# Performance work log

Hardware: AMD Instinct MI355X
Metric: run time of the kernel (lower is better)

## Reference

```python
import jax, jax.numpy as jnp
import numpy as np

B, T, D, U = 64, 128, 1024, 1024


def setup_inputs() -> dict:
    key = jax.random.key(0)
    k_x, k_r, k_s, k_wi, k_wh = jax.random.split(key, 5)
    x = jax.random.normal(k_x, (B, T, D), dtype=jnp.float32)
    reset = jax.random.randint(k_r, (B, T), 0, 2, dtype=jnp.int32)
    state = jax.random.normal(k_s, (B, T, U), dtype=jnp.float32)
    # hk.GRU params: w_i (input->3*hidden), w_h (hidden->3*hidden), bias (3*hidden)
    w_i = jax.random.normal(k_wi, (D, 3 * U), dtype=jnp.float32) * (1.0 / np.sqrt(D))
    w_h = jax.random.normal(k_wh, (U, 3 * U), dtype=jnp.float32) * (1.0 / np.sqrt(U))
    b = jnp.zeros((3 * U,), dtype=jnp.float32)
    return {"x": x, "reset": reset, "state": state, "w_i": w_i, "w_h": w_h, "b": b}


def reference(x, reset, state, w_i, w_h, b):
    # _prepare_for_rnn merges (B,T)->rows and adds a length-1 time axis, so
    # hk.dynamic_unroll(ResetCore(GRU)) == one ResetCore(GRU) step over B*T rows.
    Bd, Td, Dd = x.shape
    Ud = w_h.shape[0]
    xf = x.reshape(Bd * Td, Dd)                      # [N, D]
    h = state.reshape(Bd * Td, Ud)                   # [N, U]
    should_reset = reset.reshape(Bd * Td, 1).astype(bool)
    # hk.ResetCore: replace state with initial_state (zeros) where reset is set
    h = jnp.where(should_reset, jnp.zeros_like(h), h)
    # hk.GRU step
    gates_x = xf @ w_i                               # [N, 3U]
    zr_x, a_x = gates_x[:, : 2 * Ud], gates_x[:, 2 * Ud :]
    zr = jax.nn.sigmoid(zr_x + h @ w_h[:, : 2 * Ud] + b[: 2 * Ud])
    z, r = zr[:, :Ud], zr[:, Ud:]
    a = jnp.tanh(a_x + (r * h) @ w_h[:, 2 * Ud :] + b[2 * Ud :])
    h_new = (1.0 - z) * h + z * a                    # [N, U]
    out = h_new.reshape(Bd, Td, Ud)                  # _recover_shape
    new_state = h_new.reshape(Bd, Td, Ud)            # _rnn_reshape back to (B,T,U)
    return out, new_state
```

## Files before the change

kernel.cpp:

```cpp
#include <hip/hip_runtime.h>


typedef __attribute__((ext_vector_type(8))) short short8;
typedef __attribute__((ext_vector_type(4))) short short4v;
typedef __attribute__((ext_vector_type(4))) float floatx4;
typedef __attribute__((ext_vector_type(4))) float f32x4;

#define MROWS 8192
#define KTOT 2048
#define NU 1024
#define NKT 32
#define TBUF 32768
#define TLDS (2 * TBUF)

__device__ __forceinline__ short f2bf(float f) {
  unsigned u = __builtin_bit_cast(unsigned, f);
  u += 0x7fffu + ((u >> 16) & 1u);
  return (short)(u >> 16);
}
__device__ __forceinline__ float bf2f(short s) {
  unsigned u = ((unsigned)(unsigned short)s) << 16;
  return __builtin_bit_cast(float, u);
}
__device__ __forceinline__ float sigmoid_f(float v) { return 1.f / (1.f + __expf(-v)); }
__device__ __forceinline__ float tanh_f(float v) {
  float c = fminf(fmaxf(v, -15.f), 15.f);
  float e = __expf(2.f * c);
  return (e - 1.f) / (e + 1.f);
}

typedef __attribute__((address_space(3))) void* lds_vp;
typedef const __attribute__((address_space(1))) void* gbl_vp;
__device__ __forceinline__ void gload16(const void* g, void* lds) {
  __builtin_amdgcn_global_load_lds((gbl_vp)g, (lds_vp)lds, 16, 0, 0);
}

#define MF(a, b, c) __builtin_amdgcn_mfma_f32_16x16x32_bf16(a, b, c, 0, 0, 0)
#define VMCNT(n) asm volatile("s_waitcnt vmcnt(" #n ")" ::: "memory")
#define TILE_BAR()                  \
  do {                              \
    __builtin_amdgcn_s_barrier();   \
    asm volatile("" ::: "memory");  \
  } while (0)

__global__ __launch_bounds__(256) void wt_kernel(const float* __restrict__ w_i,
                                                 const float* __restrict__ w_h,
                                                 short* __restrict__ Wc) {
  __shared__ float tile[32][33];
  const int kb = blockIdx.x * 32;
  const int nb = blockIdx.y * 32;
  const float* src = (kb < 1024) ? w_i : w_h;
  const int kbl = kb & 1023;
  const int tx = threadIdx.x & 31;
  const int ty = threadIdx.x >> 5;
#pragma unroll
  for (int r = 0; r < 32; r += 8)
    tile[ty + r][tx] = src[(size_t)(kbl + ty + r) * 3072 + nb + tx];
  __syncthreads();
#pragma unroll
  for (int r = 0; r < 32; r += 8)
    Wc[(size_t)(nb + ty + r) * KTOT + kb + tx] = f2bf(tile[tx][ty + r]);
}

__global__ __launch_bounds__(256) void xh_kernel(const float* __restrict__ x,
                                                 const int* __restrict__ reset,
                                                 const float* __restrict__ state,
                                                 short* __restrict__ xhc) {
  const size_t i4 = (size_t)blockIdx.x * blockDim.x + threadIdx.x;
  const size_t e = i4 * 4;
  const int row = (int)(e >> 10);
  const int d = (int)(e & 1023);
  const float hm = reset[row] ? 0.f : 1.f;
  floatx4 fx = *(const floatx4*)(x + e);
  floatx4 fh = *(const floatx4*)(state + e);
  short4v cx, ch;
#pragma unroll
  for (int k = 0; k < 4; ++k) { cx[k] = f2bf(fx[k]); ch[k] = f2bf(fh[k] * hm); }
  *(short4v*)(xhc + (size_t)row * KTOT + d) = cx;
  *(short4v*)(xhc + (size_t)row * KTOT + 1024 + d) = ch;
}

__global__ __launch_bounds__(256, 2) void zr_kernel(
    const short* __restrict__ xhc, const short* __restrict__ Wc,
    const float* __restrict__ bias, float* __restrict__ zbuf,
    short* __restrict__ rh) {
  extern __shared__ char lds[];
  const int tid = threadIdx.x;
  const int wave = tid >> 6, lane = tid & 63;
  const int wm = wave >> 1, wn = wave & 1;
  const int lrow = lane & 15;
  const int g16 = (lane >> 4) << 4;
  const int swz = (lrow & 7) << 4;
  const int srow = lane >> 3;
  const int scol = ((lane & 7) ^ srow) * 8;

  const int bid = blockIdx.x;
  const int ntile = (bid & 7) | ((bid >> 9) << 3);
  const int mtile = (bid >> 3) & 63;
  const int m0 = mtile * 128, n0g = ntile * 128;

  const short* aS = xhc + (size_t)(m0 + wave * 32 + srow) * KTOT + scol;
  const short* bS = Wc + (size_t)(n0g + wave * 32 + srow) * KTOT + scol;
  const int dA = wave * 4096;
  const int dB = 16384 + wave * 4096;

  f32x4 acc[4][4];
#pragma unroll
  for (int i = 0; i < 4; ++i)
#pragma unroll
    for (int j = 0; j < 4; ++j) acc[i][j] = (f32x4){0.f, 0.f, 0.f, 0.f};

#define ZR_STAGE(t, bufp)                                                  \
  _Pragma("unroll") for (int g = 0; g < 4; ++g) {                          \
    gload16(aS + (size_t)g * 8 * KTOT + (t) * 64, (bufp) + dA + g * 1024); \
    gload16(bS + (size_t)g * 8 * KTOT + (t) * 64, (bufp) + dB + g * 1024); \
  }

  ZR_STAGE(0, lds);
  VMCNT(0);
  TILE_BAR();

  for (int t = 0; t < NKT; ++t) {
    char* buf = lds + (t & 1) * TBUF;
    if (t < NKT - 1) {
      char* nb = lds + ((t + 1) & 1) * TBUF;
      ZR_STAGE(t + 1, nb);
    }
#pragma unroll
    for (int ks = 0; ks < 2; ++ks) {
      const int colb = ((ks * 64 + g16) ^ swz);
      const char* pA = buf + (wm * 64 + lrow) * 128 + colb;
      const char* pB = buf + 16384 + (wn * 64 + lrow) * 128 + colb;
      short8 af[4], bq[4];
#pragma unroll
      for (int i = 0; i < 4; ++i) af[i] = *(const short8*)(pA + i * 2048);
#pragma unroll
      for (int j = 0; j < 4; ++j) bq[j] = *(const short8*)(pB + j * 2048);
      __builtin_amdgcn_s_setprio(1);
#pragma unroll
      for (int i = 0; i < 4; ++i)
#pragma unroll
        for (int j = 0; j < 4; ++j) acc[i][j] = MF(af[i], bq[j], acc[i][j]);
      __builtin_amdgcn_s_setprio(0);
    }
    VMCNT(0);
    TILE_BAR();
  }
#undef ZR_STAGE

  const bool zh = (n0g < 1024);
#pragma unroll
  for (int j = 0; j < 4; ++j) {
    const int gcn = n0g + wn * 64 + j * 16 + lrow;
    const float bv = bias[gcn];
#pragma unroll
    for (int i = 0; i < 4; ++i) {
#pragma unroll
      for (int rg = 0; rg < 4; ++rg) {
        const int gr = m0 + wm * 64 + i * 16 + (lane >> 4) * 4 + rg;
        const float sv = sigmoid_f(acc[i][j][rg] + bv);
        if (zh) {
          zbuf[(size_t)gr * NU + gcn] = sv;
        } else {
          const int u = gcn - 1024;
          const float hv = bf2f(xhc[(size_t)gr * KTOT + 1024 + u]);
          rh[(size_t)gr * NU + u] = f2bf(sv * hv);
        }
      }
    }
  }
}

__global__ __launch_bounds__(256, 2) void cand_kernel(
    const short* __restrict__ xhc, const short* __restrict__ rh,
    const short* __restrict__ Wc, const float* __restrict__ bias,
    const float* zbuf, float* out) {
  extern __shared__ char lds[];
  const int tid = threadIdx.x;
  const int wave = tid >> 6, lane = tid & 63;
  const int wm = wave >> 1, wn = wave & 1;
  const int lrow = lane & 15;
  const int g16 = (lane >> 4) << 4;
  const int swz = (lrow & 7) << 4;
  const int srow = lane >> 3;
  const int scol = ((lane & 7) ^ srow) * 8;

  const int bid = blockIdx.x;
  const int ntile = bid & 7;
  const int mtile = bid >> 3;
  const int m0 = mtile * 128, n0g = ntile * 128;

  const short* aX = xhc + (size_t)(m0 + wave * 32 + srow) * KTOT + scol;
  const short* aR = rh + (size_t)(m0 + wave * 32 + srow) * NU + scol;
  const short* bS = Wc + (size_t)(2048 + n0g + wave * 32 + srow) * KTOT + scol;
  const int dA = wave * 4096;
  const int dB = 16384 + wave * 4096;

  f32x4 acc[4][4];
#pragma unroll
  for (int i = 0; i < 4; ++i)
#pragma unroll
    for (int j = 0; j < 4; ++j) acc[i][j] = (f32x4){0.f, 0.f, 0.f, 0.f};

#define CD_STAGE(t, bufp)                                                        \
  _Pragma("unroll") for (int g = 0; g < 4; ++g) {                                \
    if ((t) < 16)                                                                \
      gload16(aX + (size_t)g * 8 * KTOT + (t) * 64, (bufp) + dA + g * 1024);     \
    else                                                                         \
      gload16(aR + (size_t)g * 8 * NU + ((t) - 16) * 64, (bufp) + dA + g * 1024);\
    gload16(bS + (size_t)g * 8 * KTOT + (t) * 64, (bufp) + dB + g * 1024);       \
  }

  CD_STAGE(0, lds);
  VMCNT(0);
  TILE_BAR();

  for (int t = 0; t < NKT; ++t) {
    char* buf = lds + (t & 1) * TBUF;
    if (t < NKT - 1) {
      char* nb = lds + ((t + 1) & 1) * TBUF;
      CD_STAGE(t + 1, nb);
    }
#pragma unroll
    for (int ks = 0; ks < 2; ++ks) {
      const int colb = ((ks * 64 + g16) ^ swz);
      const char* pA = buf + (wm * 64 + lrow) * 128 + colb;
      const char* pB = buf + 16384 + (wn * 64 + lrow) * 128 + colb;
      short8 af[4], bq[4];
#pragma unroll
      for (int i = 0; i < 4; ++i) af[i] = *(const short8*)(pA + i * 2048);
#pragma unroll
      for (int j = 0; j < 4; ++j) bq[j] = *(const short8*)(pB + j * 2048);
      __builtin_amdgcn_s_setprio(1);
#pragma unroll
      for (int i = 0; i < 4; ++i)
#pragma unroll
        for (int j = 0; j < 4; ++j) acc[i][j] = MF(af[i], bq[j], acc[i][j]);
      __builtin_amdgcn_s_setprio(0);
    }
    VMCNT(0);
    TILE_BAR();
  }
#undef CD_STAGE

#pragma unroll
  for (int j = 0; j < 4; ++j) {
    const int gc = n0g + wn * 64 + j * 16 + lrow;
    const float ba = bias[2048 + gc];
#pragma unroll
    for (int i = 0; i < 4; ++i) {
#pragma unroll
      for (int rg = 0; rg < 4; ++rg) {
        const int gr = m0 + wm * 64 + i * 16 + (lane >> 4) * 4 + rg;
        const float av = tanh_f(acc[i][j][rg] + ba);
        const float zv = zbuf[(size_t)gr * NU + gc];
        const float hv = bf2f(xhc[(size_t)gr * KTOT + 1024 + gc]);
        const float hn = (1.f - zv) * hv + zv * av;
        out[(size_t)gr * NU + gc] = hn;
        out[(size_t)MROWS * NU + (size_t)gr * NU + gc] = hn;
      }
    }
  }
}

extern "C" void kernel_launch(void* const* d_in, const int* in_sizes, int n_in,
                              void* d_out, int out_size, void* d_ws, size_t ws_size,
                              hipStream_t stream) {
  const float* x = (const float*)d_in[0];
  const int* reset = (const int*)d_in[1];
  const float* state = (const float*)d_in[2];
  const float* w_i = (const float*)d_in[3];
  const float* w_h = (const float*)d_in[4];
  const float* bias = (const float*)d_in[5];
  float* out = (float*)d_out;

  short* Wc = (short*)d_ws;
  short* xhc = Wc + (size_t)3072 * KTOT;
  short* rh = xhc + (size_t)MROWS * KTOT;
  float* zbuf = out + (size_t)MROWS * NU;

  hipFuncSetAttribute(reinterpret_cast<const void*>(zr_kernel),
                      hipFuncAttributeMaxDynamicSharedMemorySize, TLDS);
  hipFuncSetAttribute(reinterpret_cast<const void*>(cand_kernel),
                      hipFuncAttributeMaxDynamicSharedMemorySize, TLDS);

  wt_kernel<<<dim3(KTOT / 32, 3072 / 32), 256, 0, stream>>>(w_i, w_h, Wc);
  xh_kernel<<<dim3(MROWS * 1024 / 4 / 256), 256, 0, stream>>>(x, reset, state, xhc);

  zr_kernel<<<dim3(1024), 256, TLDS, stream>>>(xhc, Wc, bias, zbuf, rh);
  cand_kernel<<<dim3(512), 256, TLDS, stream>>>(xhc, rh, Wc, bias, zbuf, out);
}
```

Baseline: 188.5 us.

## Deepen GEMM prefetch to two tiles ahead and remap blocks per XCD

Both GEMM kernels now keep two K-tiles of global-to-LDS loads in flight. Each iteration loads the whole tile into registers, waits on LDS, barriers, then issues the t+2 prefetch into the freed buffer before running the MFMAs. The wait before each barrier changes from vmcnt(0) to vmcnt(8), so global load latency overlaps compute across a full iteration. Block-to-tile mapping now gives each XCD a contiguous band of M tiles, for better L2 reuse of A rows. The cost is an extra barrier per iteration and more registers for the fragments.

Result: faster. 162.3 us (-13.9%).

```diff
diff --git a/kernel.cpp b/kernel.cpp
--- a/kernel.cpp
+++ b/kernel.cpp
@@ -37,6 +37,7 @@
 
 #define MF(a, b, c) __builtin_amdgcn_mfma_f32_16x16x32_bf16(a, b, c, 0, 0, 0)
 #define VMCNT(n) asm volatile("s_waitcnt vmcnt(" #n ")" ::: "memory")
+#define LGKM0() asm volatile("s_waitcnt lgkmcnt(0)" ::: "memory")
 #define TILE_BAR()                  \
   do {                              \
     __builtin_amdgcn_s_barrier();   \
@@ -94,9 +95,9 @@
   const int srow = lane >> 3;
   const int scol = ((lane & 7) ^ srow) * 8;
 
-  const int bid = blockIdx.x;
-  const int ntile = (bid & 7) | ((bid >> 9) << 3);
-  const int mtile = (bid >> 3) & 63;
+  const int xcd = blockIdx.x & 7, bi = blockIdx.x >> 3;
+  const int mtile = xcd * 8 + (bi & 7);
+  const int ntile = bi >> 3;
   const int m0 = mtile * 128, n0g = ntile * 128;
 
   const short* aS = xhc + (size_t)(m0 + wave * 32 + srow) * KTOT + scol;
@@ -117,33 +118,37 @@
   }
 
   ZR_STAGE(0, lds);
-  VMCNT(0);
+  ZR_STAGE(1, lds + TBUF);
+  VMCNT(8);
   TILE_BAR();
 
+#pragma unroll 2
   for (int t = 0; t < NKT; ++t) {
     char* buf = lds + (t & 1) * TBUF;
-    if (t < NKT - 1) {
-      char* nb = lds + ((t + 1) & 1) * TBUF;
-      ZR_STAGE(t + 1, nb);
-    }
+    short8 af[2][4], bq[2][4];
 #pragma unroll
     for (int ks = 0; ks < 2; ++ks) {
       const int colb = ((ks * 64 + g16) ^ swz);
       const char* pA = buf + (wm * 64 + lrow) * 128 + colb;
       const char* pB = buf + 16384 + (wn * 64 + lrow) * 128 + colb;
-      short8 af[4], bq[4];
-#pragma unroll
-      for (int i = 0; i < 4; ++i) af[i] = *(const short8*)(pA + i * 2048);
-#pragma unroll
-      for (int j = 0; j < 4; ++j) bq[j] = *(const short8*)(pB + j * 2048);
-      __builtin_amdgcn_s_setprio(1);
+#pragma unroll
+      for (int i = 0; i < 4; ++i) af[ks][i] = *(const short8*)(pA + i * 2048);
+#pragma unroll
+      for (int j = 0; j < 4; ++j) bq[ks][j] = *(const short8*)(pB + j * 2048);
+    }
+    LGKM0();
+    TILE_BAR();
+    if (t + 2 < NKT) { ZR_STAGE(t + 2, buf); }
+    __builtin_amdgcn_s_setprio(1);
+#pragma unroll
+    for (int ks = 0; ks < 2; ++ks)
 #pragma unroll
       for (int i = 0; i < 4; ++i)
 #pragma unroll
-        for (int j = 0; j < 4; ++j) acc[i][j] = MF(af[i], bq[j], acc[i][j]);
-      __builtin_amdgcn_s_setprio(0);
-    }
-    VMCNT(0);
+        for (int j = 0; j < 4; ++j)
+          acc[i][j] = MF(af[ks][i], bq[ks][j], acc[i][j]);
+    __builtin_amdgcn_s_setprio(0);
+    if (t + 2 < NKT) { VMCNT(8); } else { VMCNT(0); }
     TILE_BAR();
   }
 #undef ZR_STAGE
@@ -185,9 +190,9 @@
   const int srow = lane >> 3;
   const int scol = ((lane & 7) ^ srow) * 8;
 
-  const int bid = blockIdx.x;
-  const int ntile = bid & 7;
-  const int mtile = bid >> 3;
+  const int xcd = blockIdx.x & 7, bi = blockIdx.x >> 3;
+  const int mtile = xcd * 8 + (bi & 7);
+  const int ntile = bi >> 3;
   const int m0 = mtile * 128, n0g = ntile * 128;
 
   const short* aX = xhc + (size_t)(m0 + wave * 32 + srow) * KTOT + scol;
@@ -212,33 +217,37 @@
   }
 
   CD_STAGE(0, lds);
-  VMCNT(0);
+  CD_STAGE(1, lds + TBUF);
+  VMCNT(8);
   TILE_BAR();
 
+#pragma unroll 2
   for (int t = 0; t < NKT; ++t) {
     char* buf = lds + (t & 1) * TBUF;
-    if (t < NKT - 1) {
-      char* nb = lds + ((t + 1) & 1) * TBUF;
-      CD_STAGE(t + 1, nb);
-    }
+    short8 af[2][4], bq[2][4];
 #pragma unroll
     for (int ks = 0; ks < 2; ++ks) {
       const int colb = ((ks * 64 + g16) ^ swz);
       const char* pA = buf + (wm * 64 + lrow) * 128 + colb;
       const char* pB = buf + 16384 + (wn * 64 + lrow) * 128 + colb;
-      short8 af[4], bq[4];
-#pragma unroll
-      for (int i = 0; i < 4; ++i) af[i] = *(const short8*)(pA + i * 2048);
-#pragma unroll
-      for (int j = 0; j < 4; ++j) bq[j] = *(const short8*)(pB + j * 2048);
-      __builtin_amdgcn_s_setprio(1);
+#pragma unroll
+      for (int i = 0; i < 4; ++i) af[ks][i] = *(const short8*)(pA + i * 2048);
+#pragma unroll
+      for (int j = 0; j < 4; ++j) bq[ks][j] = *(const short8*)(pB + j * 2048);
+    }
+    LGKM0();
+    TILE_BAR();
+    if (t + 2 < NKT) { CD_STAGE(t + 2, buf); }
+    __builtin_amdgcn_s_setprio(1);
+#pragma unroll
+    for (int ks = 0; ks < 2; ++ks)
 #pragma unroll
       for (int i = 0; i < 4; ++i)
 #pragma unroll
-        for (int j = 0; j < 4; ++j) acc[i][j] = MF(af[i], bq[j], acc[i][j]);
-      __builtin_amdgcn_s_setprio(0);
-    }
-    VMCNT(0);
+        for (int j = 0; j < 4; ++j)
+          acc[i][j] = MF(af[ks][i], bq[ks][j], acc[i][j]);
+    __builtin_amdgcn_s_setprio(0);
+    if (t + 2 < NKT) { VMCNT(8); } else { VMCNT(0); }
     TILE_BAR();
   }
 #undef CD_STAGE
```
